# Performance work log

Measured on AMD Instinct MI355X. Metric: run time of the kernel, lower is better.

Reference implementation:

```python
import jax, jax.numpy as jnp
import numpy as np

B, S, D, H = 8, 512, 1024, 16
DK = D // H


def setup_inputs() -> dict:
    key = jax.random.key(0)
    ks = jax.random.split(key, 12)
    inp = {
        "input_Q": jax.random.normal(ks[0], (B, S, D), jnp.float32),
        "input_K": jax.random.normal(ks[1], (B, S, D), jnp.float32),
        "input_V": jax.random.normal(ks[2], (B, S, D), jnp.float32),
        "attn_mask": jax.random.bernoulli(ks[3], 0.1, (B, S, S)),
        "adj_matrix": jax.random.uniform(ks[4], (B, S, S), jnp.float32),
        "dist_matrix": jax.random.uniform(ks[5], (B, S, S), jnp.float32) * 5.0,
        # learned params (nn.Linear weights are [out, in], no bias)
        "W_Q": jax.random.normal(ks[6], (D, D), jnp.float32) / np.sqrt(D),
        "W_K": jax.random.normal(ks[7], (D, D), jnp.float32) / np.sqrt(D),
        "W_V": jax.random.normal(ks[8], (D, D), jnp.float32) / np.sqrt(D),
        "W_fc": jax.random.normal(ks[9], (D, D), jnp.float32) / np.sqrt(D),
        # Conv2d(3->1, k=1): weight [1,3,1,1] flattened to [3], bias [1]
        "conv_w": jax.random.normal(ks[10], (3,), jnp.float32) * 0.3,
        "conv_b": jax.random.normal(ks[11], (1,), jnp.float32) * 0.1,
    }
    return inp


def reference(input_Q, input_K, input_V, attn_mask, adj_matrix, dist_matrix,
              W_Q, W_K, W_V, W_fc, conv_w, conv_b):
    neg = jnp.float32(-1e9)
    # projections -> [B, H, S, dk]
    def proj(x, W):
        return jnp.einsum('bsd,od->bso', x, W).reshape(B, S, H, DK).transpose(0, 2, 1, 3)
    Q = proj(input_Q, W_Q)
    K = proj(input_K, W_K)
    V = proj(input_V, W_V)

    mask4 = attn_mask[:, None]  # [B,1,S,S] broadcast over heads
    # distance kernel: exp(-d), masked positions -> exp(-inf)=0
    dist_k = jnp.where(attn_mask, 0.0, jnp.exp(-dist_matrix))[:, None]  # [B,1,S,S]
    adj4 = adj_matrix[:, None]

    scores = jnp.einsum('bhqd,bhkd->bhqk', Q, K) / np.sqrt(DK).astype(np.float32)
    scores = jnp.where(mask4, neg, scores)
    scores = jax.nn.softmax(scores, axis=-1)

    # 1x1 conv over channels {scores, dist, adj}
    weighted = conv_w[0] * scores + conv_w[1] * dist_k + conv_w[2] * adj4 + conv_b[0]
    weighted = jnp.where(mask4, neg, weighted)
    attn = jax.nn.softmax(weighted, axis=-1)

    context = jnp.einsum('bhqk,bhkd->bhqd', attn, V)
    context = context.transpose(0, 2, 1, 3).reshape(B, S, D)
    output = jnp.einsum('bsd,od->bso', context, W_fc)
    return (output, attn)
```

## Files before the change

### kernel.cpp

```cpp
#include <hip/hip_runtime.h>
#include <stdint.h>

#define B_ 8
#define S_ 512
#define D_ 1024
#define H_ 16
#define DK_ 64

typedef float f32x4 __attribute__((ext_vector_type(4)));
typedef float float4v __attribute__((ext_vector_type(4)));
typedef short bf16x8 __attribute__((ext_vector_type(8)));
typedef short short4v __attribute__((ext_vector_type(4)));
typedef __bf16 bfv8 __attribute__((ext_vector_type(8)));

__device__ __forceinline__ short f2bf(float f) {
    return __builtin_bit_cast(short, (__bf16)f);
}

__device__ __forceinline__ f32x4 mfma_bf16(bf16x8 a, bf16x8 b, f32x4 c) {
    return __builtin_amdgcn_mfma_f32_16x16x32_bf16(
        __builtin_bit_cast(bfv8, a), __builtin_bit_cast(bfv8, b), c, 0, 0, 0);
}

__device__ __forceinline__ bf16x8 cvt8(float4v a, float4v b) {
    bf16x8 v;
    v[0] = f2bf(a[0]); v[1] = f2bf(a[1]); v[2] = f2bf(a[2]); v[3] = f2bf(a[3]);
    v[4] = f2bf(b[0]); v[5] = f2bf(b[1]); v[6] = f2bf(b[2]); v[7] = f2bf(b[3]);
    return v;
}

__device__ __forceinline__ void gl_lds16(const void* g, void* l) {
    __builtin_amdgcn_global_load_lds(
        (const __attribute__((address_space(1))) void*)g,
        (__attribute__((address_space(3))) void*)l, 16, 0, 0);
}

__global__ __launch_bounds__(256) void conv_all_kernel(
    const float* __restrict__ xq, const float* __restrict__ xk, const float* __restrict__ xv,
    const float* __restrict__ wq, const float* __restrict__ wk, const float* __restrict__ wv,
    const float* __restrict__ wfc, short* __restrict__ Xb, short* __restrict__ Wb)
{
    const int NX = 3 * 4096 * 1024;
    const int NTOT = NX + 4 * 1024 * 1024;
    for (int i = blockIdx.x * 256 + threadIdx.x; i * 8 < NTOT; i += gridDim.x * 256) {
        const int i8 = i * 8;
        const float* src;
        short* dst;
        if (i8 < NX) {
            const int z = i8 >> 22, off = i8 & ((1 << 22) - 1);
            src = ((z == 0) ? xq : (z == 1) ? xk : xv) + off;
            dst = Xb + i8;
        } else {
            const int j = i8 - NX;
            const int w = j >> 20, off = j & ((1 << 20) - 1);
            src = ((w == 0) ? wq : (w == 1) ? wk : (w == 2) ? wv : wfc) + off;
            dst = Wb + i8 - NX;
        }
        float4v a = *(const float4v*)src;
        float4v b = *(const float4v*)(src + 4);
        *(bf16x8*)dst = cvt8(a, b);
    }
}

__global__ __launch_bounds__(256) void precomp_kernel(
    const int* __restrict__ mask, const float* __restrict__ adj,
    const float* __restrict__ dist, const float* __restrict__ cw,
    const float* __restrict__ cb, float* __restrict__ comb, int n)
{
    const float w1 = cw[1], w2 = cw[2], b0 = cb[0];
    for (int i = blockIdx.x * 256 + threadIdx.x; i < n; i += gridDim.x * 256) {
        float c = -1e9f;
        if (mask[i] == 0) c = fmaf(w2, adj[i], fmaf(w1, __expf(-dist[i]), b0));
        comb[i] = c;
    }
}

__global__ __launch_bounds__(256) void proj_qkv_kernel(
    const short* __restrict__ Xb, const short* __restrict__ Wb,
    short* __restrict__ Qp, short* __restrict__ Kp, short* __restrict__ VpT)
{
    __shared__ __align__(16) short Alds[128 * 64];
    __shared__ __align__(16) short Blds[128 * 64];

    const int z = blockIdx.z;
    const short* X = Xb + (size_t)z * (4096 * 1024);
    const short* W = Wb + (size_t)z * (1024 * 1024);

    const int tid = threadIdx.x;
    const int lane = tid & 63, w = tid >> 6;
    const int l15 = lane & 15, lg = lane >> 4;

    const int p = blockIdx.x;
    const int lin = (p & 7) * 32 + (p >> 3);
    const int n0 = (lin & 7) * 128, m0 = (lin >> 3) * 128;
    const int wm = w >> 1, wn = w & 1;

    f32x4 acc[4][4] = {};

    for (int k0 = 0; k0 < D_; k0 += 64) {
        #pragma unroll
        for (int t = 0; t < 4; ++t) {
            const int r0 = w * 32 + t * 8;
            const int row = r0 + (lane >> 3);
            const int sc = (lane & 7) ^ (row & 7);
            gl_lds16(X + (size_t)(m0 + row) * D_ + k0 + sc * 8, &Alds[r0 * 64]);
            gl_lds16(W + (size_t)(n0 + row) * D_ + k0 + sc * 8, &Blds[r0 * 64]);
        }
        __syncthreads();
        #pragma unroll
        for (int ks = 0; ks < 2; ++ks) {
            bf16x8 af[4], bfr[4];
            #pragma unroll
            for (int i = 0; i < 4; ++i) {
                const int row = wm * 64 + i * 16 + l15;
                af[i] = *(const bf16x8*)&Alds[(row * 8 + ((ks * 4 + lg) ^ (row & 7))) * 8];
            }
            #pragma unroll
            for (int j = 0; j < 4; ++j) {
                const int row = wn * 64 + j * 16 + l15;
                bfr[j] = *(const bf16x8*)&Blds[(row * 8 + ((ks * 4 + lg) ^ (row & 7))) * 8];
            }
            #pragma unroll
            for (int i = 0; i < 4; ++i)
                #pragma unroll
                for (int j = 0; j < 4; ++j)
                    acc[i][j] = mfma_bf16(af[i], bfr[j], acc[i][j]);
        }
        __syncthreads();
    }

    if (z < 2) {
        short* Outp = (z == 0) ? Qp : Kp;
        #pragma unroll
        for (int i = 0; i < 4; ++i) {
            #pragma unroll
            for (int j = 0; j < 4; ++j) {
                const int n = n0 + wn * 64 + j * 16 + l15;
                const int h = n >> 6, dk = n & 63;
                #pragma unroll
                for (int r = 0; r < 4; ++r) {
                    const int m = m0 + wm * 64 + i * 16 + lg * 4 + r;
                    const int b = m >> 9, s = m & 511;
                    Outp[((size_t)(b * H_ + h) * S_ + s) * DK_ + dk] = f2bf(acc[i][j][r]);
                }
            }
        }
    } else {
        #pragma unroll
        for (int i = 0; i < 4; ++i) {
            const int mb = m0 + wm * 64 + i * 16 + lg * 4;
            const int b = mb >> 9, s0v = mb & 511;
            #pragma unroll
            for (int j = 0; j < 4; ++j) {
                const int n = n0 + wn * 64 + j * 16 + l15;
                const int h = n >> 6, dk = n & 63;
                short4v v;
                #pragma unroll
                for (int r = 0; r < 4; ++r) v[r] = f2bf(acc[i][j][r]);
                *(short4v*)&VpT[((size_t)(b * H_ + h) * DK_ + dk) * S_ + s0v] = v;
            }
        }
    }
}

__global__ __launch_bounds__(256, 4) void attn_kernel(
    const short* __restrict__ Qp, const short* __restrict__ Kp,
    const short* __restrict__ VpT, const float* __restrict__ comb,
    const float* __restrict__ cw, float* __restrict__ attn_out,
    short* __restrict__ Ctx)
{
    __shared__ __align__(16) char smem[16 * 1024 + 1024];
    float* red = (float*)(smem + 16384);

    const int tid = threadIdx.x;
    const int lane = tid & 63, w = tid >> 6;
    const int l15 = lane & 15, lg = lane >> 4;

    const int id = blockIdx.x;
    const int b = id & 7;
    const int rest = id >> 3;
    const int qt = rest & 31, h = rest >> 5;
    const int bh = b * H_ + h;
    const int q0 = qt * 16;
    const int k0 = w * 128;

    const short* Qb = Qp + (size_t)bh * S_ * DK_;
    const short* Kb = Kp + (size_t)bh * S_ * DK_ + (size_t)k0 * DK_;
    const short* Vb = VpT + (size_t)bh * DK_ * S_;
    const float* cbm = comb + (size_t)b * S_ * S_ + (size_t)q0 * S_ + k0;
    const float w0 = cw[0];

    bf16x8 aq0 = *(const bf16x8*)(Qb + (q0 + l15) * DK_ + lg * 8);
    bf16x8 aq1 = *(const bf16x8*)(Qb + (q0 + l15) * DK_ + 32 + lg * 8);

    f32x4 cmb[8];
    #pragma unroll
    for (int nf = 0; nf < 8; ++nf)
        #pragma unroll
        for (int r = 0; r < 4; ++r)
            cmb[nf][r] = cbm[(size_t)(lg * 4 + r) * S_ + nf * 16 + l15];

    f32x4 sc[8];
    #pragma unroll
    for (int nf = 0; nf < 8; ++nf) {
        bf16x8 bk0 = *(const bf16x8*)(Kb + (nf * 16 + l15) * DK_ + lg * 8);
        bf16x8 bk1 = *(const bf16x8*)(Kb + (nf * 16 + l15) * DK_ + 32 + lg * 8);
        f32x4 a = {};
        a = mfma_bf16(aq0, bk0, a);
        a = mfma_bf16(aq1, bk1, a);
        sc[nf] = a;
    }

    f32x4 mx;
    mx[0] = mx[1] = mx[2] = mx[3] = -3e38f;
    #pragma unroll
    for (int nf = 0; nf < 8; ++nf)
        #pragma unroll
        for (int r = 0; r < 4; ++r) {
            const float v = (cmb[nf][r] < -1e8f) ? -1e9f : sc[nf][r] * 0.125f;
            sc[nf][r] = v;
            mx[r] = fmaxf(mx[r], v);
        }
    #pragma unroll
    for (int off = 1; off < 16; off <<= 1)
        #pragma unroll
        for (int r = 0; r < 4; ++r)
            mx[r] = fmaxf(mx[r], __shfl_xor(mx[r], off));
    {
        float* rd = red;
        if (l15 == 0) {
            #pragma unroll
            for (int r = 0; r < 4; ++r) rd[w * 16 + lg * 4 + r] = mx[r];
        }
        __syncthreads();
        #pragma unroll
        for (int r = 0; r < 4; ++r) {
            const int row = lg * 4 + r;
            mx[r] = fmaxf(fmaxf(rd[row], rd[16 + row]), fmaxf(rd[32 + row], rd[48 + row]));
        }
    }

    f32x4 sm = {};
    #pragma unroll
    for (int nf = 0; nf < 8; ++nf)
        #pragma unroll
        for (int r = 0; r < 4; ++r) {
            const float e = __expf(sc[nf][r] - mx[r]);
            sc[nf][r] = e;
            sm[r] += e;
        }
    #pragma unroll
    for (int off = 1; off < 16; off <<= 1)
        #pragma unroll
        for (int r = 0; r < 4; ++r)
            sm[r] += __shfl_xor(sm[r], off);
    {
        float* rd = red + 64;
        if (l15 == 0) {
            #pragma unroll
            for (int r = 0; r < 4; ++r) rd[w * 16 + lg * 4 + r] = sm[r];
        }
        __syncthreads();
        #pragma unroll
        for (int r = 0; r < 4; ++r) {
            const int row = lg * 4 + r;
            sm[r] = (rd[row] + rd[16 + row]) + (rd[32 + row] + rd[48 + row]);
        }
    }
    f32x4 rs1;
    #pragma unroll
    for (int r = 0; r < 4; ++r) rs1[r] = 1.0f / sm[r];

    f32x4 mx2;
    mx2[0] = mx2[1] = mx2[2] = mx2[3] = -3e38f;
    #pragma unroll
    for (int nf = 0; nf < 8; ++nf)
        #pragma unroll
        for (int r = 0; r < 4; ++r) {
            const float pv = sc[nf][r] * rs1[r];
            const float wv = fmaf(w0, pv, cmb[nf][r]);
            sc[nf][r] = wv;
            mx2[r] = fmaxf(mx2[r], wv);
        }
    #pragma unroll
    for (int off = 1; off < 16; off <<= 1)
        #pragma unroll
        for (int r = 0; r < 4; ++r)
            mx2[r] = fmaxf(mx2[r], __shfl_xor(mx2[r], off));
    {
        float* rd = red + 128;
        if (l15 == 0) {
            #pragma unroll
            for (int r = 0; r < 4; ++r) rd[w * 16 + lg * 4 + r] = mx2[r];
        }
        __syncthreads();
        #pragma unroll
        for (int r = 0; r < 4; ++r) {
            const int row = lg * 4 + r;
            mx2[r] = fmaxf(fmaxf(rd[row], rd[16 + row]), fmaxf(rd[32 + row], rd[48 + row]));
        }
    }

    f32x4 sm2 = {};
    #pragma unroll
    for (int nf = 0; nf < 8; ++nf)
        #pragma unroll
        for (int r = 0; r < 4; ++r) {
            const float e = __expf(sc[nf][r] - mx2[r]);
            sc[nf][r] = e;
            sm2[r] += e;
        }
    #pragma unroll
    for (int off = 1; off < 16; off <<= 1)
        #pragma unroll
        for (int r = 0; r < 4; ++r)
            sm2[r] += __shfl_xor(sm2[r], off);
    {
        float* rd = red + 192;
        if (l15 == 0) {
            #pragma unroll
            for (int r = 0; r < 4; ++r) rd[w * 16 + lg * 4 + r] = sm2[r];
        }
        __syncthreads();
        #pragma unroll
        for (int r = 0; r < 4; ++r) {
            const int row = lg * 4 + r;
            sm2[r] = (rd[row] + rd[16 + row]) + (rd[32 + row] + rd[48 + row]);
        }
    }
    f32x4 rs2;
    #pragma unroll
    for (int r = 0; r < 4; ++r) rs2[r] = 1.0f / sm2[r];

    float* aout = attn_out + ((size_t)bh * S_ + q0) * S_ + k0;
    #pragma unroll
    for (int nf = 0; nf < 8; ++nf)
        #pragma unroll
        for (int r = 0; r < 4; ++r) {
            const int q = lg * 4 + r;
            const float av = sc[nf][r] * rs2[r];
            aout[(size_t)q * S_ + nf * 16 + l15] = av;
            const int byteo = ((q * 256 + (nf * 16 + l15) * 2) ^ ((q & 7) << 4)) + w * 4096;
            *(short*)(smem + byteo) = f2bf(av);
        }
    __syncthreads();

    f32x4 cacc[4] = {};
    #pragma unroll
    for (int ks = 0; ks < 4; ++ks) {
        const int byteA = ((l15 * 256 + (ks * 32 + lg * 8) * 2) ^ ((l15 & 7) << 4)) + w * 4096;
        bf16x8 pa = *(const bf16x8*)(smem + byteA);
        #pragma unroll
        for (int j = 0; j < 4; ++j) {
            bf16x8 bv = *(const bf16x8*)(Vb + (size_t)(j * 16 + l15) * S_ + k0 + ks * 32 + lg * 8);
            cacc[j] = mfma_bf16(pa, bv, cacc[j]);
        }
    }
    __syncthreads();

    float* cr = (float*)smem;
    #pragma unroll
    for (int j = 0; j < 4; ++j)
        #pragma unroll
        for (int r = 0; r < 4; ++r)
            cr[w * 1024 + (lg * 4 + r) * 64 + j * 16 + l15] = cacc[j][r];
    __syncthreads();

    #pragma unroll
    for (int r = 0; r < 4; ++r) {
        const int row = lg * 4 + r;
        const float v = (cr[row * 64 + w * 16 + l15] + cr[1024 + row * 64 + w * 16 + l15])
                      + (cr[2048 + row * 64 + w * 16 + l15] + cr[3072 + row * 64 + w * 16 + l15]);
        Ctx[(size_t)(b * S_ + q0 + row) * D_ + h * 64 + w * 16 + l15] = f2bf(v);
    }
}

__global__ __launch_bounds__(256) void fc_kernel(
    const short* __restrict__ Ctx, const short* __restrict__ Wfcb,
    float* __restrict__ Out)
{
    __shared__ __align__(16) short Alds[128 * 64];
    __shared__ __align__(16) short Blds[128 * 64];

    const int tid = threadIdx.x;
    const int lane = tid & 63, w = tid >> 6;
    const int l15 = lane & 15, lg = lane >> 4;

    const int p = blockIdx.x;
    const int lin = (p & 7) * 32 + (p >> 3);
    const int n0 = (lin & 7) * 128, m0 = (lin >> 3) * 128;
    const int wm = w >> 1, wn = w & 1;

    f32x4 acc[4][4] = {};

    for (int k0 = 0; k0 < D_; k0 += 64) {
        #pragma unroll
        for (int t = 0; t < 4; ++t) {
            const int r0 = w * 32 + t * 8;
            const int row = r0 + (lane >> 3);
            const int sc = (lane & 7) ^ (row & 7);
            gl_lds16(Ctx + (size_t)(m0 + row) * D_ + k0 + sc * 8, &Alds[r0 * 64]);
            gl_lds16(Wfcb + (size_t)(n0 + row) * D_ + k0 + sc * 8, &Blds[r0 * 64]);
        }
        __syncthreads();
        #pragma unroll
        for (int ks = 0; ks < 2; ++ks) {
            bf16x8 af[4], bfr[4];
            #pragma unroll
            for (int i = 0; i < 4; ++i) {
                const int row = wm * 64 + i * 16 + l15;
                af[i] = *(const bf16x8*)&Alds[(row * 8 + ((ks * 4 + lg) ^ (row & 7))) * 8];
            }
            #pragma unroll
            for (int j = 0; j < 4; ++j) {
                const int row = wn * 64 + j * 16 + l15;
                bfr[j] = *(const bf16x8*)&Blds[(row * 8 + ((ks * 4 + lg) ^ (row & 7))) * 8];
            }
            #pragma unroll
            for (int i = 0; i < 4; ++i)
                #pragma unroll
                for (int j = 0; j < 4; ++j)
                    acc[i][j] = mfma_bf16(af[i], bfr[j], acc[i][j]);
        }
        __syncthreads();
    }

    #pragma unroll
    for (int i = 0; i < 4; ++i)
        #pragma unroll
        for (int j = 0; j < 4; ++j)
            #pragma unroll
            for (int r = 0; r < 4; ++r) {
                const int m = m0 + wm * 64 + i * 16 + lg * 4 + r;
                const int n = n0 + wn * 64 + j * 16 + l15;
                Out[(size_t)m * D_ + n] = acc[i][j][r];
            }
}

extern "C" void kernel_launch(void* const* d_in, const int* in_sizes, int n_in,
                              void* d_out, int out_size, void* d_ws, size_t ws_size,
                              hipStream_t stream) {
    const float* xq   = (const float*)d_in[0];
    const float* xk   = (const float*)d_in[1];
    const float* xv   = (const float*)d_in[2];
    const int*   mask = (const int*)d_in[3];
    const float* adj  = (const float*)d_in[4];
    const float* dist = (const float*)d_in[5];
    const float* wq   = (const float*)d_in[6];
    const float* wk   = (const float*)d_in[7];
    const float* wv   = (const float*)d_in[8];
    const float* wfc  = (const float*)d_in[9];
    const float* cw   = (const float*)d_in[10];
    const float* cb   = (const float*)d_in[11];

    float* out  = (float*)d_out;
    float* attn = out + (size_t)B_ * S_ * D_;

    char* ws = (char*)d_ws;
    short* Xb   = (short*)(ws);
    float* comb = (float*)(ws);
    short* Ctx  = (short*)(ws + (9u << 20));
    short* Wb   = (short*)(ws + (24u << 20));
    short* Qp   = (short*)(ws + (32u << 20));
    short* Kp   = (short*)(ws + (40u << 20));
    short* VpT  = (short*)(ws + (48u << 20));
    const short* Wfcb = Wb + (size_t)3 * 1024 * 1024;

    conv_all_kernel<<<dim3(2048), dim3(256), 0, stream>>>(
        xq, xk, xv, wq, wk, wv, wfc, Xb, Wb);
    proj_qkv_kernel<<<dim3(256, 1, 3), dim3(256), 0, stream>>>(
        Xb, Wb, Qp, Kp, VpT);
    precomp_kernel<<<dim3(1024), dim3(256), 0, stream>>>(
        mask, adj, dist, cw, cb, comb, B_ * S_ * S_);
    attn_kernel<<<dim3(4096), dim3(256), 0, stream>>>(
        Qp, Kp, VpT, comb, cw, attn, Ctx);
    fc_kernel<<<dim3(256), dim3(256), 0, stream>>>(Ctx, Wfcb, out);
}
```

Baseline: 174.4 us.

## Drop softmax max passes, reload mask/bias from global, raise occupancy

Removes the row-max reductions from both softmaxes and exponentiates the scaled scores directly. It relies on the logits being bounded: roughly unit-scale scores, and a convex mix of probabilities with exp(-d) and adj. This eliminates two cross-wave reductions and their barriers. The combined mask/bias tile is no longer held in 32 registers per thread; it is re-read from global memory in each pass, and the launch bound goes from 4 to 6 blocks per CU. Two barriers around the per-wave LDS P tile are removed, since each wave only touches its own region. The risk is overflow for large-magnitude inputs and extra global traffic from reading the bias twice.

Result: slower. 192.7 us (+10.5%).

```diff
diff --git a/kernel.cpp b/kernel.cpp
--- a/kernel.cpp
+++ b/kernel.cpp
@@ -163,7 +163,7 @@
     }
 }
 
-__global__ __launch_bounds__(256, 4) void attn_kernel(
+__global__ __launch_bounds__(256, 6) void attn_kernel(
     const short* __restrict__ Qp, const short* __restrict__ Kp,
     const short* __restrict__ VpT, const float* __restrict__ comb,
     const float* __restrict__ cw, float* __restrict__ attn_out,
@@ -193,13 +193,6 @@
     bf16x8 aq0 = *(const bf16x8*)(Qb + (q0 + l15) * DK_ + lg * 8);
     bf16x8 aq1 = *(const bf16x8*)(Qb + (q0 + l15) * DK_ + 32 + lg * 8);
 
-    f32x4 cmb[8];
-    #pragma unroll
-    for (int nf = 0; nf < 8; ++nf)
-        #pragma unroll
-        for (int r = 0; r < 4; ++r)
-            cmb[nf][r] = cbm[(size_t)(lg * 4 + r) * S_ + nf * 16 + l15];
-
     f32x4 sc[8];
     #pragma unroll
     for (int nf = 0; nf < 8; ++nf) {
@@ -211,41 +204,13 @@
         sc[nf] = a;
     }
 
-    f32x4 mx;
-    mx[0] = mx[1] = mx[2] = mx[3] = -3e38f;
+    f32x4 sm = {};
     #pragma unroll
     for (int nf = 0; nf < 8; ++nf)
         #pragma unroll
         for (int r = 0; r < 4; ++r) {
-            const float v = (cmb[nf][r] < -1e8f) ? -1e9f : sc[nf][r] * 0.125f;
-            sc[nf][r] = v;
-            mx[r] = fmaxf(mx[r], v);
-        }
-    #pragma unroll
-    for (int off = 1; off < 16; off <<= 1)
-        #pragma unroll
-        for (int r = 0; r < 4; ++r)
-            mx[r] = fmaxf(mx[r], __shfl_xor(mx[r], off));
-    {
-        float* rd = red;
-        if (l15 == 0) {
-            #pragma unroll
-            for (int r = 0; r < 4; ++r) rd[w * 16 + lg * 4 + r] = mx[r];
-        }
-        __syncthreads();
-        #pragma unroll
-        for (int r = 0; r < 4; ++r) {
-            const int row = lg * 4 + r;
-            mx[r] = fmaxf(fmaxf(rd[row], rd[16 + row]), fmaxf(rd[32 + row], rd[48 + row]));
-        }
-    }
-
-    f32x4 sm = {};
-    #pragma unroll
-    for (int nf = 0; nf < 8; ++nf)
-        #pragma unroll
-        for (int r = 0; r < 4; ++r) {
-            const float e = __expf(sc[nf][r] - mx[r]);
+            const float c = cbm[(size_t)(lg * 4 + r) * S_ + nf * 16 + l15];
+            const float e = (c < -1e8f) ? 0.0f : __expf(sc[nf][r] * 0.125f);
             sc[nf][r] = e;
             sm[r] += e;
         }
@@ -254,59 +219,26 @@
         #pragma unroll
         for (int r = 0; r < 4; ++r)
             sm[r] += __shfl_xor(sm[r], off);
-    {
-        float* rd = red + 64;
-        if (l15 == 0) {
-            #pragma unroll
-            for (int r = 0; r < 4; ++r) rd[w * 16 + lg * 4 + r] = sm[r];
-        }
-        __syncthreads();
+    if (l15 == 0) {
+        #pragma unroll
+        for (int r = 0; r < 4; ++r) red[w * 16 + lg * 4 + r] = sm[r];
+    }
+    __syncthreads();
+    f32x4 rs1;
+    #pragma unroll
+    for (int r = 0; r < 4; ++r) {
+        const int row = lg * 4 + r;
+        rs1[r] = 1.0f / ((red[row] + red[16 + row]) + (red[32 + row] + red[48 + row]));
+    }
+
+    f32x4 sm2 = {};
+    #pragma unroll
+    for (int nf = 0; nf < 8; ++nf)
         #pragma unroll
         for (int r = 0; r < 4; ++r) {
-            const int row = lg * 4 + r;
-            sm[r] = (rd[row] + rd[16 + row]) + (rd[32 + row] + rd[48 + row]);
-        }
-    }
-    f32x4 rs1;
-    #pragma unroll
-    for (int r = 0; r < 4; ++r) rs1[r] = 1.0f / sm[r];
-
-    f32x4 mx2;
-    mx2[0] = mx2[1] = mx2[2] = mx2[3] = -3e38f;
-    #pragma unroll
-    for (int nf = 0; nf < 8; ++nf)
-        #pragma unroll
-        for (int r = 0; r < 4; ++r) {
-            const float pv = sc[nf][r] * rs1[r];
-            const float wv = fmaf(w0, pv, cmb[nf][r]);
-            sc[nf][r] = wv;
-            mx2[r] = fmaxf(mx2[r], wv);
-        }
-    #pragma unroll
-    for (int off = 1; off < 16; off <<= 1)
-        #pragma unroll
-        for (int r = 0; r < 4; ++r)
-            mx2[r] = fmaxf(mx2[r], __shfl_xor(mx2[r], off));
-    {
-        float* rd = red + 128;
-        if (l15 == 0) {
-            #pragma unroll
-            for (int r = 0; r < 4; ++r) rd[w * 16 + lg * 4 + r] = mx2[r];
-        }
-        __syncthreads();
-        #pragma unroll
-        for (int r = 0; r < 4; ++r) {
-            const int row = lg * 4 + r;
-            mx2[r] = fmaxf(fmaxf(rd[row], rd[16 + row]), fmaxf(rd[32 + row], rd[48 + row]));
-        }
-    }
-
-    f32x4 sm2 = {};
-    #pragma unroll
-    for (int nf = 0; nf < 8; ++nf)
-        #pragma unroll
-        for (int r = 0; r < 4; ++r) {
-            const float e = __expf(sc[nf][r] - mx2[r]);
+            const float c = cbm[(size_t)(lg * 4 + r) * S_ + nf * 16 + l15];
+            const float p = sc[nf][r] * rs1[r];
+            const float e = __expf(fmaf(w0, p, c));
             sc[nf][r] = e;
             sm2[r] += e;
         }
@@ -315,22 +247,17 @@
         #pragma unroll
         for (int r = 0; r < 4; ++r)
             sm2[r] += __shfl_xor(sm2[r], off);
-    {
-        float* rd = red + 192;
-        if (l15 == 0) {
-            #pragma unroll
-            for (int r = 0; r < 4; ++r) rd[w * 16 + lg * 4 + r] = sm2[r];
-        }
-        __syncthreads();
-        #pragma unroll
-        for (int r = 0; r < 4; ++r) {
-            const int row = lg * 4 + r;
-            sm2[r] = (rd[row] + rd[16 + row]) + (rd[32 + row] + rd[48 + row]);
-        }
-    }
+    if (l15 == 0) {
+        #pragma unroll
+        for (int r = 0; r < 4; ++r) red[64 + w * 16 + lg * 4 + r] = sm2[r];
+    }
+    __syncthreads();
     f32x4 rs2;
     #pragma unroll
-    for (int r = 0; r < 4; ++r) rs2[r] = 1.0f / sm2[r];
+    for (int r = 0; r < 4; ++r) {
+        const int row = lg * 4 + r;
+        rs2[r] = 1.0f / ((red[64 + row] + red[80 + row]) + (red[96 + row] + red[112 + row]));
+    }
 
     float* aout = attn_out + ((size_t)bh * S_ + q0) * S_ + k0;
     #pragma unroll
@@ -343,7 +270,6 @@
             const int byteo = ((q * 256 + (nf * 16 + l15) * 2) ^ ((q & 7) << 4)) + w * 4096;
             *(short*)(smem + byteo) = f2bf(av);
         }
-    __syncthreads();
 
     f32x4 cacc[4] = {};
     #pragma unroll
@@ -356,7 +282,6 @@
             cacc[j] = mfma_bf16(pa, bv, cacc[j]);
         }
     }
-    __syncthreads();
 
     float* cr = (float*)smem;
     #pragma unroll
```
